# Kernel optimization log

Hardware: AMD Instinct MI355X
Metric: run time of the kernel (lower is better)

## Reference

```python
import math
import jax, jax.numpy as jnp
import numpy as np

B, S, H, M, E = 4, 4096, 1024, 1024, 16
CAPACITY_FACTOR = 2.0
ROUTE_SCALE = 1.0


def setup_inputs() -> dict:
    key = jax.random.key(0)
    ks = jax.random.split(key, 8)
    return {
        "hidden_states": jax.random.normal(ks[0], (B, S, H), dtype=jnp.float32),
        "hidden_states_unmodulated": jax.random.normal(ks[1], (B, S, H), dtype=jnp.float32),
        "timestep": jax.random.normal(ks[2], (B, H), dtype=jnp.float32),
        "gate_w": jax.random.normal(ks[3], (2 * H, E), dtype=jnp.float32) * 0.02,
        "gate_up_proj": jax.random.normal(ks[4], (E, H, 2 * M), dtype=jnp.float32) * 0.02,
        "down_proj": jax.random.normal(ks[5], (E, M, H), dtype=jnp.float32) * 0.02,
        "shared_gate_up_w": jax.random.normal(ks[6], (H, 2 * M), dtype=jnp.float32) * 0.02,
        "shared_down_w": jax.random.normal(ks[7], (M, H), dtype=jnp.float32) * 0.02,
    }


def reference(hidden_states, hidden_states_unmodulated, timestep, gate_w,
              gate_up_proj, down_proj, shared_gate_up_w, shared_down_w):
    b, s, h = hidden_states.shape
    e = gate_up_proj.shape[0]
    capacity = max(1, math.ceil(CAPACITY_FACTOR * s / e))  # static per shapes

    # --- router ---
    t = jnp.broadcast_to(timestep[:, None, :], (b, s, h))
    router_input = jnp.concatenate([t, hidden_states_unmodulated], axis=-1)  # [b,s,2h]
    logits = router_input @ gate_w                                           # [b,s,e]
    scores = jax.nn.sigmoid(logits.astype(jnp.float32)).astype(logits.dtype)
    affinity = jnp.swapaxes(scores, 1, 2)                                    # [b,e,s]

    # --- expert-choice top-k ---
    gating, top_idx = jax.lax.top_k(affinity, capacity)                      # [b,e,cap]
    offsets = (jnp.arange(b) * s)[:, None, None]
    gidx = jnp.swapaxes(offsets + top_idx, 0, 1).reshape(-1)                 # [e*b*cap]
    gflat = jnp.swapaxes(gating, 0, 1).reshape(-1)

    # normalize per-token scores over experts that picked the token
    sums = jnp.zeros(b * s, dtype=gflat.dtype).at[gidx].add(gflat)
    gflat = gflat / (sums[gidx] + 1e-12) * ROUTE_SCALE

    # --- dispatch + grouped SwiGLU experts ---
    x_flat = hidden_states.reshape(b * s, h)
    routed = x_flat[gidx].reshape(e, b * capacity, h)
    gu = jnp.einsum('eth,ehf->etf', routed, gate_up_proj)                    # [e,t,2m]
    g, u = jnp.split(gu, 2, axis=-1)
    expert_out = jnp.einsum('etm,emh->eth', jax.nn.silu(g) * u, down_proj)
    expert_out = expert_out.reshape(e * b * capacity, h)
    expert_out = (expert_out.astype(jnp.float32) *
                  gflat.astype(jnp.float32)[:, None]).astype(hidden_states.dtype)

    # --- shared expert (SwiGLUProj order: hidden * silu(gate)) ---
    hgu = hidden_states @ shared_gate_up_w                                   # [b,s,2m]
    hs_, hg = jnp.split(hgu, 2, axis=-1)
    shared = (hs_ * jax.nn.silu(hg)) @ shared_down_w                         # [b,s,h]

    # --- scatter combine ---
    out = shared.reshape(b * s, h).at[gidx].add(expert_out)
    return out.reshape(b, s, h)
```

## Files before the change

### kernel.cpp

```cpp
#include <hip/hip_runtime.h>
#include <math.h>

#define Bb 4
#define Ss 4096
#define Hh 1024
#define Mm 1024
#define Ee 16
#define CAPk 512

typedef unsigned short u16;
typedef __attribute__((ext_vector_type(8))) short short8;
typedef __attribute__((ext_vector_type(4))) float floatx4;
typedef __attribute__((ext_vector_type(4))) unsigned short ushort4v;

__device__ __forceinline__ float silu_f(float x) {
    return x / (1.0f + expf(-x));
}

__device__ __forceinline__ u16 f2b(float x) {
    union { float f; unsigned u; } v; v.f = x;
    unsigned r = (v.u + 0x7fffu + ((v.u >> 16) & 1u)) >> 16;
    return (u16)r;
}

__device__ __forceinline__ void gl_lds16(const void* g, void* l) {
    __builtin_amdgcn_global_load_lds((const __attribute__((address_space(1))) void*)g,
                                     (__attribute__((address_space(3))) void*)l, 16, 0, 0);
}


__global__ __launch_bounds__(256)
void conv_router(const float* __restrict__ hidden, u16* __restrict__ Xb,
                 const float* __restrict__ hsu,
                 const float* __restrict__ gate_w,
                 const float* __restrict__ timestep,
                 float* __restrict__ scores) {
    const int t = threadIdx.x;
    if (blockIdx.x >= 256) {
        int i = ((blockIdx.x - 256) * 256 + t) * 4;
        float4 v = *(const float4*)(hidden + i);
        ushort4v o = { f2b(v.x), f2b(v.y), f2b(v.z), f2b(v.w) };
        *(ushort4v*)(Xb + i) = o;
        return;
    }
    __shared__ float Xs[64 * 64];
    __shared__ float Gs[64 * 16];
    const int rbid = blockIdx.x;
    const int row0 = rbid * 64;
    const int b = row0 >> 12;
    const int wave = t >> 6, lane = t & 63;
    const int e0 = wave * 4;
    const float* gw2 = gate_w + (size_t)Hh * Ee;

    float tl0 = 0.f, tl1 = 0.f, tl2 = 0.f, tl3 = 0.f;
    {
        const float* tsrow = timestep + (size_t)b * Hh;
#pragma unroll
        for (int j = 0; j < 16; ++j) {
            int h = lane + 64 * j;
            float tv = tsrow[h];
            const float* gw = gate_w + (size_t)h * Ee + e0;
            tl0 += tv * gw[0]; tl1 += tv * gw[1]; tl2 += tv * gw[2]; tl3 += tv * gw[3];
        }
#pragma unroll
        for (int off = 32; off; off >>= 1) {
            tl0 += __shfl_xor(tl0, off); tl1 += __shfl_xor(tl1, off);
            tl2 += __shfl_xor(tl2, off); tl3 += __shfl_xor(tl3, off);
        }
    }

    float acc0 = 0.f, acc1 = 0.f, acc2 = 0.f, acc3 = 0.f;

    for (int k0 = 0; k0 < Hh; k0 += 64) {
        __syncthreads();
#pragma unroll
        for (int r = 0; r < 4; ++r) {
            int tok = r * 16 + (t >> 4);
            int cslot = t & 15;
            int g = cslot ^ (tok & 15);
            const float* src = hsu + (size_t)(row0 + tok) * Hh + k0 + g * 4;
            char* dst = (char*)Xs + r * 4096 + wave * 1024;
            gl_lds16(src, dst);
        }
        {
            const float* src = gw2 + (size_t)k0 * Ee + t * 4;
            char* dst = (char*)Gs + wave * 1024;
            gl_lds16(src, dst);
        }
        __syncthreads();
#pragma unroll
        for (int kk = 0; kk < 64; kk += 4) {
            int slot = (kk >> 2) ^ (lane & 15);
            float4 a = *(const float4*)&Xs[lane * 64 + slot * 4];
            float4 g0 = *(const float4*)&Gs[(kk + 0) * Ee + e0];
            float4 g1 = *(const float4*)&Gs[(kk + 1) * Ee + e0];
            float4 g2 = *(const float4*)&Gs[(kk + 2) * Ee + e0];
            float4 g3 = *(const float4*)&Gs[(kk + 3) * Ee + e0];
            acc0 += a.x * g0.x; acc0 += a.y * g1.x; acc0 += a.z * g2.x; acc0 += a.w * g3.x;
            acc1 += a.x * g0.y; acc1 += a.y * g1.y; acc1 += a.z * g2.y; acc1 += a.w * g3.y;
            acc2 += a.x * g0.z; acc2 += a.y * g1.z; acc2 += a.z * g2.z; acc2 += a.w * g3.z;
            acc3 += a.x * g0.w; acc3 += a.y * g1.w; acc3 += a.z * g2.w; acc3 += a.w * g3.w;
        }
    }
    const int s = (row0 + lane) & (Ss - 1);
    float l0 = acc0 + tl0;
    float l1 = acc1 + tl1;
    float l2 = acc2 + tl2;
    float l3 = acc3 + tl3;
    scores[((size_t)(b * Ee + e0 + 0)) * Ss + s] = 1.f / (1.f + expf(-l0));
    scores[((size_t)(b * Ee + e0 + 1)) * Ss + s] = 1.f / (1.f + expf(-l1));
    scores[((size_t)(b * Ee + e0 + 2)) * Ss + s] = 1.f / (1.f + expf(-l2));
    scores[((size_t)(b * Ee + e0 + 3)) * Ss + s] = 1.f / (1.f + expf(-l3));
}

__global__ __launch_bounds__(1024)
void topk_kernel(const float* __restrict__ scores,
                 int* __restrict__ rank) {
    const int be = blockIdx.x;
    const float* sc = scores + (size_t)be * Ss;
    int* rk = rank + (size_t)be * Ss;
    const int t = threadIdx.x;
    const int lane = t & 63, w = t >> 6;
    __shared__ unsigned hist[256];
    __shared__ unsigned wtot[16];
    __shared__ unsigned sh_prefix;
    __shared__ int sh_need;
    __shared__ unsigned cnt_gt;

#pragma unroll
    for (int i = 0; i < 4; ++i) rk[t * 4 + i] = -1;

    unsigned vu[4];
#pragma unroll
    for (int i = 0; i < 4; ++i) vu[i] = __float_as_uint(sc[t * 4 + i]);

    unsigned prefix = 0;
    int need = CAPk;
    for (int pass = 0; pass < 4; ++pass) {
        const int shift = 24 - 8 * pass;
        if (t < 256) hist[t] = 0;
        __syncthreads();
#pragma unroll
        for (int i = 0; i < 4; ++i) {
            unsigned u = vu[i];
            bool ok = (pass == 0) || ((u >> (shift + 8)) == prefix);
            if (ok) atomicAdd(&hist[(u >> shift) & 255u], 1u);
        }
        __syncthreads();
        unsigned hval = (t < 256) ? hist[t] : 0u;
        unsigned s = hval;
#pragma unroll
        for (int d = 1; d < 64; d <<= 1) {
            unsigned o = __shfl_down(s, d);
            if (lane + d < 64) s += o;
        }
        if (lane == 0 && w < 4) wtot[w] = s;
        __syncthreads();
        if (t < 256) {
#pragma unroll
            for (int w2 = 0; w2 < 4; ++w2)
                if (w2 > w) s += wtot[w2];
            unsigned Snext = s - hval;
            if (s >= (unsigned)need && Snext < (unsigned)need) {
                sh_prefix = (prefix << 8) | (unsigned)t;
                sh_need = need - (int)Snext;
            }
        }
        __syncthreads();
        prefix = sh_prefix;
        need = sh_need;
        __syncthreads();
    }
    const unsigned T = prefix;
    const int need_eq = need;
    const unsigned ngt = (unsigned)(CAPk - need_eq);

    int myeq = 0;
#pragma unroll
    for (int i = 0; i < 4; ++i) myeq += (vu[i] == T) ? 1 : 0;
    unsigned e = (unsigned)myeq;
#pragma unroll
    for (int d = 1; d < 64; d <<= 1) {
        unsigned o = __shfl_up(e, d);
        if (lane >= d) e += o;
    }
    if (lane == 63) wtot[w] = e;
    if (t == 0) cnt_gt = 0;
    __syncthreads();
    unsigned eqr = e - (unsigned)myeq;
#pragma unroll
    for (int w2 = 0; w2 < 16; ++w2)
        if (w2 < w) eqr += wtot[w2];
#pragma unroll
    for (int i = 0; i < 4; ++i) {
        unsigned u = vu[i];
        int s = t * 4 + i;
        if (u > T) {
            unsigned slot = atomicAdd(&cnt_gt, 1u);
            rk[s] = (int)slot;
        } else if (u == T) {
            if ((int)eqr < need_eq) {
                rk[s] = (int)(ngt + eqr);
            }
            eqr++;
        }
    }
}

__global__ __launch_bounds__(256)
void route_build(const float* __restrict__ scores, const int* __restrict__ rank,
                 int* __restrict__ slot_token, float* __restrict__ slot_w,
                 int* __restrict__ cnt, int* __restrict__ inv) {
    const int token = blockIdx.x * 256 + threadIdx.x;
    const int b = token >> 12, s = token & (Ss - 1);
    int rr[16];
    float gg[16];
    float sum = 0.f;
#pragma unroll
    for (int e = 0; e < 16; ++e) {
        size_t idx = (size_t)(b * Ee + e) * Ss + s;
        int r = rank[idx];
        rr[e] = r;
        float g = (r >= 0) ? scores[idx] : 0.f;
        gg[e] = g;
        sum += g;
    }
    int pos = 0;
#pragma unroll
    for (int e = 0; e < 16; ++e) {
        if (rr[e] >= 0) {
            float wv = gg[e] / (sum + 1e-12f);
            int o = (e * Bb + b) * CAPk + rr[e];
            slot_token[o] = token;
            slot_w[o] = wv;
            inv[token * 16 + pos] = o;
            ++pos;
        }
    }
    cnt[token] = pos;
}

__global__ __launch_bounds__(256)
void combine_kernel(const int* __restrict__ cnt, const int* __restrict__ inv,
                    const float* __restrict__ eo, float* __restrict__ out) {
    const int token = blockIdx.x;
    const int k = cnt[token];
    if (k == 0) return;
    const int col = threadIdx.x * 4;
    const size_t rowoff = (size_t)token * 1024 + col;
    float4 acc = *(const float4*)(out + rowoff);
    for (int j = 0; j < k; ++j) {
        int slot = inv[token * 16 + j];
        float4 v = *(const float4*)(eo + (size_t)slot * 1024 + col);
        acc.x += v.x; acc.y += v.y; acc.z += v.z; acc.w += v.w;
    }
    *(float4*)(out + rowoff) = acc;
}


__device__ __forceinline__ void tpose_body(const float* __restrict__ Ws, u16* __restrict__ Wd,
                                           int N, int n0, int k0, float tile[64][65], int t) {
    int lr = t >> 4, lc = (t & 15) * 4;
#pragma unroll
    for (int i = 0; i < 4; ++i) {
        float4 v = *(const float4*)&Ws[(size_t)(k0 + lr + i * 16) * N + n0 + lc];
        tile[lr + i * 16][lc + 0] = v.x;
        tile[lr + i * 16][lc + 1] = v.y;
        tile[lr + i * 16][lc + 2] = v.z;
        tile[lr + i * 16][lc + 3] = v.w;
    }
    __syncthreads();
    int on = t >> 2;
    int ok0 = (t & 3) * 16;
    u16 buf[16];
#pragma unroll
    for (int j = 0; j < 16; ++j) buf[j] = f2b(tile[ok0 + j][on]);
    u16* dp = &Wd[(size_t)(n0 + on) * 1024 + k0 + ok0];
    *(short8*)(dp) = *(short8*)&buf[0];
    *(short8*)(dp + 8) = *(short8*)&buf[8];
}

__global__ __launch_bounds__(256)
void transpose_bf16(const float* __restrict__ W, u16* __restrict__ Wt,
                    int N, size_t zsrc, size_t zdst) {
    __shared__ float tile[64][65];
    int n0 = blockIdx.x * 64, k0 = blockIdx.y * 64, z = blockIdx.z;
    tpose_body(W + (size_t)z * zsrc, Wt + (size_t)z * zdst, N, n0, k0, tile, threadIdx.x);
}

__global__ __launch_bounds__(256)
void transpose_all(const float* __restrict__ gate_up, const float* __restrict__ down,
                   const float* __restrict__ sh_gu, const float* __restrict__ sh_dn,
                   u16* __restrict__ Wt1r, u16* __restrict__ Wt2r,
                   u16* __restrict__ Wt1s, u16* __restrict__ Wt2s) {
    __shared__ float tile[64][65];
    const int id = blockIdx.x;
    const float* Ws; u16* Wd; int N, n0, k0;
    if (id < 8192) {
        int z = id >> 9, r = id & 511;
        n0 = (r & 31) * 64; k0 = (r >> 5) * 64; N = 2048;
        Ws = gate_up + (size_t)z * 2097152; Wd = Wt1r + (size_t)z * 2097152;
    } else if (id < 12288) {
        int i2 = id - 8192; int z = i2 >> 8, r = i2 & 255;
        n0 = (r & 15) * 64; k0 = (r >> 4) * 64; N = 1024;
        Ws = down + (size_t)z * 1048576; Wd = Wt2r + (size_t)z * 1048576;
    } else if (id < 12800) {
        int r = id - 12288;
        n0 = (r & 31) * 64; k0 = (r >> 5) * 64; N = 2048;
        Ws = sh_gu; Wd = Wt1s;
    } else {
        int r = id - 12800;
        n0 = (r & 15) * 64; k0 = (r >> 4) * 64; N = 1024;
        Ws = sh_dn; Wd = Wt2s;
    }
    tpose_body(Ws, Wd, N, n0, k0, tile, threadIdx.x);
}


__device__ __forceinline__ void stage_tile512(const u16* __restrict__ grow, int k0,
                                              u16* lds, int t) {
#pragma unroll
    for (int r = 0; r < 2; ++r) {
        int ci = r * 512 + t;
        int m = ci >> 3;
        int c = (ci & 7) ^ (m & 7);
        const u16* src = grow + (size_t)m * 1024 + k0 + c * 8;
        u16* dst = lds + ((r * 8192 + (t >> 6) * 1024) >> 1);
        gl_lds16(src, dst);
    }
}

__device__ __forceinline__ void stage_rows512(const u16* __restrict__ A, const int* rid,
                                              int k0, u16* lds, int t) {
#pragma unroll
    for (int r = 0; r < 2; ++r) {
        int ci = r * 512 + t;
        int m = ci >> 3;
        int c = (ci & 7) ^ (m & 7);
        const u16* src = A + (size_t)rid[r] * 1024 + k0 + c * 8;
        u16* dst = lds + ((r * 8192 + (t >> 6) * 1024) >> 1);
        gl_lds16(src, dst);
    }
}

template <bool SILU_FIRST, bool GATHER>
__global__ __launch_bounds__(512, 4)
void gemm1_flat(const u16* __restrict__ A,
                const u16* __restrict__ W1t, u16* __restrict__ act,
                const int* __restrict__ slot_token, int p0, int p1) {
    __shared__ u16 lA[128 * 64];
    __shared__ u16 lB1[128 * 64];
    __shared__ u16 lB2[128 * 64];
    const int t = threadIdx.x;
    const int L = blockIdx.x;
    const int x = L & 7, j = L >> 3;
    int z = 0, bm0, n0;
    if (GATHER) {
        if (p1 == 8) { z = p0 + x; bm0 = (j >> 3) << 7; }
        else         { z = p0 + (x >> 1); bm0 = (((x & 1) << 3) + (j >> 3)) << 7; }
    } else {
        bm0 = (p0 + x * (p1 >> 3) + (j >> 3)) << 7;
    }
    n0 = (j & 7) << 7;
    const int out_base = (GATHER ? z * 2048 : 0) + bm0;
    const u16* B1row = W1t + ((size_t)(GATHER ? z * 2048 : 0) + n0) * 1024;
    const u16* B2row = B1row + (size_t)1024 * 1024;
    const int lane = t & 63;
    const int wv = t >> 6;
    const int wm = wv & 1, wn = wv >> 1;
    const int quad = lane >> 4, l15 = lane & 15;

    int rid[2];
#pragma unroll
    for (int r = 0; r < 2; ++r) {
        int m = (t >> 3) + 64 * r;
        rid[r] = GATHER ? slot_token[z * (Bb * CAPk) + bm0 + m] : (bm0 + m);
    }

    floatx4 zero4 = {0.f, 0.f, 0.f, 0.f};
    floatx4 acc1[4][2], acc2[4][2];
#pragma unroll
    for (int i = 0; i < 4; ++i)
#pragma unroll
        for (int j2 = 0; j2 < 2; ++j2) { acc1[i][j2] = zero4; acc2[i][j2] = zero4; }

    for (int k0 = 0; k0 < 1024; k0 += 64) {
        __syncthreads();
        stage_rows512(A, rid, k0, lA, t);
        stage_tile512(B1row, k0, lB1, t);
        stage_tile512(B2row, k0, lB2, t);
        __syncthreads();
#pragma unroll
        for (int kc = 0; kc < 2; ++kc) {
            short8 af[4], bf1[2], bf2[2];
#pragma unroll
            for (int mi = 0; mi < 4; ++mi) {
                int m = wm * 64 + mi * 16 + l15;
                int off = m * 64 + (((kc * 4 + quad) ^ (m & 7)) * 8);
                af[mi] = *(const short8*)&lA[off];
            }
#pragma unroll
            for (int ni = 0; ni < 2; ++ni) {
                int n = wn * 32 + ni * 16 + l15;
                int off = n * 64 + (((kc * 4 + quad) ^ (n & 7)) * 8);
                bf1[ni] = *(const short8*)&lB1[off];
                bf2[ni] = *(const short8*)&lB2[off];
            }
#pragma unroll
            for (int mi = 0; mi < 4; ++mi)
#pragma unroll
                for (int ni = 0; ni < 2; ++ni) {
                    acc1[mi][ni] = __builtin_amdgcn_mfma_f32_16x16x32_bf16(af[mi], bf1[ni], acc1[mi][ni], 0, 0, 0);
                    acc2[mi][ni] = __builtin_amdgcn_mfma_f32_16x16x32_bf16(af[mi], bf2[ni], acc2[mi][ni], 0, 0, 0);
                }
        }
    }
#pragma unroll
    for (int mi = 0; mi < 4; ++mi)
#pragma unroll
        for (int ni = 0; ni < 2; ++ni)
#pragma unroll
            for (int r = 0; r < 4; ++r) {
                int m = wm * 64 + mi * 16 + quad * 4 + r;
                int n = wn * 32 + ni * 16 + l15;
                float c1 = acc1[mi][ni][r], c2 = acc2[mi][ni][r];
                float v = SILU_FIRST ? silu_f(c1) * c2 : c1 * silu_f(c2);
                act[(size_t)(out_base + m) * 1024 + n0 + n] = f2b(v);
            }
}

template <int MODE>
__global__ __launch_bounds__(512, 4)
void gemm2_flat(const u16* __restrict__ A,
                const u16* __restrict__ W2t, const float* __restrict__ slot_w,
                float* __restrict__ outp, int p0, int p1) {
    __shared__ u16 lA[128 * 64];
    __shared__ u16 lB[128 * 64];
    __shared__ float s_w[(MODE == 2) ? 128 : 1];
    const int t = threadIdx.x;
    const int L = blockIdx.x;
    const int x = L & 7, j = L >> 3;
    int z = 0, bm0, n0;
    if (MODE == 2) {
        if (p1 == 8) { z = p0 + x; bm0 = (j >> 3) << 7; }
        else         { z = p0 + (x >> 1); bm0 = (((x & 1) << 3) + (j >> 3)) << 7; }
    } else {
        bm0 = (p0 + x * (p1 >> 3) + (j >> 3)) << 7;
    }
    n0 = (j & 7) << 7;
    const int row_base = (MODE == 2 ? z * 2048 : 0) + bm0;
    const u16* Arow = A + (size_t)row_base * 1024;
    const u16* Brow = W2t + ((size_t)(MODE == 2 ? z * 1024 : 0) + n0) * 1024;
    const int lane = t & 63;
    const int wv = t >> 6;
    const int wm = wv & 1, wn = wv >> 1;
    const int quad = lane >> 4, l15 = lane & 15;

    if (MODE == 2 && t < 128) {
        s_w[t] = slot_w[row_base + t];
    }

    floatx4 zero4 = {0.f, 0.f, 0.f, 0.f};
    floatx4 acc[4][2];
#pragma unroll
    for (int i = 0; i < 4; ++i)
#pragma unroll
        for (int j2 = 0; j2 < 2; ++j2) acc[i][j2] = zero4;

    for (int k0 = 0; k0 < 1024; k0 += 64) {
        __syncthreads();
        stage_tile512(Arow, k0, lA, t);
        stage_tile512(Brow, k0, lB, t);
        __syncthreads();
#pragma unroll
        for (int kc = 0; kc < 2; ++kc) {
            short8 af[4], bf[2];
#pragma unroll
            for (int mi = 0; mi < 4; ++mi) {
                int m = wm * 64 + mi * 16 + l15;
                int off = m * 64 + (((kc * 4 + quad) ^ (m & 7)) * 8);
                af[mi] = *(const short8*)&lA[off];
            }
#pragma unroll
            for (int ni = 0; ni < 2; ++ni) {
                int n = wn * 32 + ni * 16 + l15;
                int off = n * 64 + (((kc * 4 + quad) ^ (n & 7)) * 8);
                bf[ni] = *(const short8*)&lB[off];
            }
#pragma unroll
            for (int mi = 0; mi < 4; ++mi)
#pragma unroll
                for (int ni = 0; ni < 2; ++ni)
                    acc[mi][ni] = __builtin_amdgcn_mfma_f32_16x16x32_bf16(af[mi], bf[ni], acc[mi][ni], 0, 0, 0);
        }
    }
#pragma unroll
    for (int mi = 0; mi < 4; ++mi)
#pragma unroll
        for (int ni = 0; ni < 2; ++ni)
#pragma unroll
            for (int r = 0; r < 4; ++r) {
                int m = wm * 64 + mi * 16 + quad * 4 + r;
                int n = wn * 32 + ni * 16 + l15;
                float c = acc[mi][ni][r];
                if (MODE == 2) {
                    outp[(size_t)(row_base + m) * 1024 + n0 + n] = c * s_w[m];
                } else {
                    outp[(size_t)(row_base + m) * 1024 + n0 + n] = c;
                }
            }
}


template <bool SILU_FIRST, bool GATHER>
__global__ __launch_bounds__(512, 4)
void gemm1_mfma(const u16* __restrict__ A, int a_row0, int zstride,
                const u16* __restrict__ W1t, u16* __restrict__ act,
                const int* __restrict__ slot_token, int e_base) {
    __shared__ u16 lA[128 * 64];
    __shared__ u16 lB1[128 * 64];
    __shared__ u16 lB2[128 * 64];
    const int t = threadIdx.x;
    const int n0 = blockIdx.x * 128;
    const int bm0 = blockIdx.y * 128;
    const int z = blockIdx.z;
    const int zb = z * zstride;
    const u16* B1row = W1t + ((size_t)z * 2048 + n0) * 1024;
    const u16* B2row = B1row + (size_t)1024 * 1024;
    const int lane = t & 63;
    const int wv = t >> 6;
    const int wm = wv & 1, wn = wv >> 1;
    const int quad = lane >> 4, l15 = lane & 15;

    int rid[2];
#pragma unroll
    for (int r = 0; r < 2; ++r) {
        int m = (t >> 3) + 64 * r;
        rid[r] = GATHER ? slot_token[(e_base + z) * (Bb * CAPk) + bm0 + m]
                        : (a_row0 + zb + bm0 + m);
    }

    floatx4 zero4 = {0.f, 0.f, 0.f, 0.f};
    floatx4 acc1[4][2], acc2[4][2];
#pragma unroll
    for (int i = 0; i < 4; ++i)
#pragma unroll
        for (int j = 0; j < 2; ++j) { acc1[i][j] = zero4; acc2[i][j] = zero4; }

    for (int k0 = 0; k0 < 1024; k0 += 64) {
        __syncthreads();
        stage_rows512(A, rid, k0, lA, t);
        stage_tile512(B1row, k0, lB1, t);
        stage_tile512(B2row, k0, lB2, t);
        __syncthreads();
#pragma unroll
        for (int kc = 0; kc < 2; ++kc) {
            short8 af[4], bf1[2], bf2[2];
#pragma unroll
            for (int mi = 0; mi < 4; ++mi) {
                int m = wm * 64 + mi * 16 + l15;
                int off = m * 64 + (((kc * 4 + quad) ^ (m & 7)) * 8);
                af[mi] = *(const short8*)&lA[off];
            }
#pragma unroll
            for (int ni = 0; ni < 2; ++ni) {
                int n = wn * 32 + ni * 16 + l15;
                int off = n * 64 + (((kc * 4 + quad) ^ (n & 7)) * 8);
                bf1[ni] = *(const short8*)&lB1[off];
                bf2[ni] = *(const short8*)&lB2[off];
            }
#pragma unroll
            for (int mi = 0; mi < 4; ++mi)
#pragma unroll
                for (int ni = 0; ni < 2; ++ni) {
                    acc1[mi][ni] = __builtin_amdgcn_mfma_f32_16x16x32_bf16(af[mi], bf1[ni], acc1[mi][ni], 0, 0, 0);
                    acc2[mi][ni] = __builtin_amdgcn_mfma_f32_16x16x32_bf16(af[mi], bf2[ni], acc2[mi][ni], 0, 0, 0);
                }
        }
    }
#pragma unroll
    for (int mi = 0; mi < 4; ++mi)
#pragma unroll
        for (int ni = 0; ni < 2; ++ni)
#pragma unroll
            for (int r = 0; r < 4; ++r) {
                int m = wm * 64 + mi * 16 + quad * 4 + r;
                int n = wn * 32 + ni * 16 + l15;
                float c1 = acc1[mi][ni][r], c2 = acc2[mi][ni][r];
                float v = SILU_FIRST ? silu_f(c1) * c2 : c1 * silu_f(c2);
                act[(size_t)(zb + bm0 + m) * 1024 + n0 + n] = f2b(v);
            }
}

template <int MODE>
__global__ __launch_bounds__(512, 4)
void gemm2_mfma(const u16* __restrict__ A, int zstride,
                const u16* __restrict__ W2t,
                const int* __restrict__ slot_token, const float* __restrict__ slot_w,
                float* __restrict__ out, int out_row0, int e_base) {
    __shared__ u16 lA[128 * 64];
    __shared__ u16 lB[128 * 64];
    __shared__ int s_tok[(MODE == 1) ? 128 : 1];
    __shared__ float s_w[(MODE == 1 || MODE == 2) ? 128 : 1];
    const int t = threadIdx.x;
    const int n0 = blockIdx.x * 128;
    const int bm0 = blockIdx.y * 128;
    const int z = blockIdx.z;
    const int zb = z * zstride;
    const u16* Arow = A + (size_t)(zb + bm0) * 1024;
    const u16* Brow = W2t + ((size_t)z * 1024 + n0) * 1024;
    const int lane = t & 63;
    const int wv = t >> 6;
    const int wm = wv & 1, wn = wv >> 1;
    const int quad = lane >> 4, l15 = lane & 15;

    if ((MODE == 1 || MODE == 2) && t < 128) {
        int gi = (e_base + z) * (Bb * CAPk) + bm0 + t;
        if (MODE == 1) s_tok[t] = slot_token[gi];
        s_w[t] = slot_w[gi];
    }

    floatx4 zero4 = {0.f, 0.f, 0.f, 0.f};
    floatx4 acc[4][2];
#pragma unroll
    for (int i = 0; i < 4; ++i)
#pragma unroll
        for (int j = 0; j < 2; ++j) acc[i][j] = zero4;

    for (int k0 = 0; k0 < 1024; k0 += 64) {
        __syncthreads();
        stage_tile512(Arow, k0, lA, t);
        stage_tile512(Brow, k0, lB, t);
        __syncthreads();
#pragma unroll
        for (int kc = 0; kc < 2; ++kc) {
            short8 af[4], bf[2];
#pragma unroll
            for (int mi = 0; mi < 4; ++mi) {
                int m = wm * 64 + mi * 16 + l15;
                int off = m * 64 + (((kc * 4 + quad) ^ (m & 7)) * 8);
                af[mi] = *(const short8*)&lA[off];
            }
#pragma unroll
            for (int ni = 0; ni < 2; ++ni) {
                int n = wn * 32 + ni * 16 + l15;
                int off = n * 64 + (((kc * 4 + quad) ^ (n & 7)) * 8);
                bf[ni] = *(const short8*)&lB[off];
            }
#pragma unroll
            for (int mi = 0; mi < 4; ++mi)
#pragma unroll
                for (int ni = 0; ni < 2; ++ni)
                    acc[mi][ni] = __builtin_amdgcn_mfma_f32_16x16x32_bf16(af[mi], bf[ni], acc[mi][ni], 0, 0, 0);
        }
    }
#pragma unroll
    for (int mi = 0; mi < 4; ++mi)
#pragma unroll
        for (int ni = 0; ni < 2; ++ni)
#pragma unroll
            for (int r = 0; r < 4; ++r) {
                int m = wm * 64 + mi * 16 + quad * 4 + r;
                int n = wn * 32 + ni * 16 + l15;
                float c = acc[mi][ni][r];
                if (MODE == 1) {
                    atomicAdd(&out[(size_t)s_tok[m] * 1024 + n0 + n], c * s_w[m]);
                } else if (MODE == 2) {
                    out[((size_t)((e_base + z) * (Bb * CAPk) + bm0 + m)) * 1024 + n0 + n] = c * s_w[m];
                } else {
                    out[(size_t)(out_row0 + bm0 + m) * 1024 + n0 + n] = c;
                }
            }
}


extern "C" void kernel_launch(void* const* d_in, const int* in_sizes, int n_in,
                              void* d_out, int out_size, void* d_ws, size_t ws_size,
                              hipStream_t stream) {
    const float* hidden   = (const float*)d_in[0];
    const float* hsu      = (const float*)d_in[1];
    const float* timestep = (const float*)d_in[2];
    const float* gate_w   = (const float*)d_in[3];
    const float* gate_up  = (const float*)d_in[4];
    const float* down     = (const float*)d_in[5];
    const float* sh_gu    = (const float*)d_in[6];
    const float* sh_dn    = (const float*)d_in[7];
    float* out = (float*)d_out;

    char* p = (char*)d_ws;
    auto alloc = [&](size_t bytes) { char* r = p; p += (bytes + 255) & ~(size_t)255; return r; };
    float* scores    = (float*)alloc((size_t)Bb * Ee * Ss * 4);
    int*   rank      = (int*)  alloc((size_t)Bb * Ee * Ss * 4);
    int*   slot_token= (int*)  alloc((size_t)Ee * Bb * CAPk * 4);
    float* slot_w    = (float*)alloc((size_t)Ee * Bb * CAPk * 4);
    int*   cnt       = (int*)  alloc((size_t)Bb * Ss * 4);
    int*   inv       = (int*)  alloc((size_t)Bb * Ss * 16 * 4);
    u16*   Xb        = (u16*)  alloc((size_t)16384 * 1024 * 2);
    char* phase = p;
    long long avail = (long long)((char*)d_ws + ws_size - phase);
    if (avail < 0) avail = 0;

    const long long eo_bytes     = (long long)32768 * 1024 * 4;
    const long long per_e        = ((long long)2048 * 1024 + 1024 * 1024 +
                                    (long long)2048 * 1024) * 2;
    const long long shared_fixed = ((long long)2048 * 1024 + 1024 * 1024) * 2;
    const long long fast_need    = ((long long)16 * 2048 * 1024 +
                                    (long long)16 * 1024 * 1024 +
                                    (long long)16 * 2048 * 1024 +
                                    (long long)2048 * 1024 +
                                    (long long)1024 * 1024) * 2;

    conv_router<<<16384 + (Bb * Ss) / 64, 256, 0, stream>>>(hidden, Xb, hsu, gate_w,
                                                            timestep, scores);
    topk_kernel<<<Bb * Ee, 1024, 0, stream>>>(scores, rank);
    route_build<<<(Bb * Ss) / 256, 256, 0, stream>>>(scores, rank, slot_token, slot_w,
                                                     cnt, inv);

    bool use_eo = (avail >= eo_bytes + (per_e > (shared_fixed + (long long)128 * 2048)
                                        ? per_e : (shared_fixed + (long long)128 * 2048)));
    bool fast   = use_eo && (avail - eo_bytes >= fast_need);

    if (fast) {
        float* eo = (float*)phase;
        char* ph2 = phase + eo_bytes;
        u16* Wt1r = (u16*)ph2;
        u16* Wt2r = Wt1r + (size_t)16 * 2048 * 1024;
        u16* actR = Wt2r + (size_t)16 * 1024 * 1024;
        u16* Wt1s = actR + (size_t)16 * 2048 * 1024;
        u16* Wt2s = Wt1s + (size_t)2048 * 1024;
        u16* actS = Wt1r;

        transpose_all<<<13056, 256, 0, stream>>>(gate_up, down, sh_gu, sh_dn,
                                                 Wt1r, Wt2r, Wt1s, Wt2s);
        for (int e0 = 0; e0 < 16; e0 += 4)
            gemm1_flat<true, true><<<512, 512, 0, stream>>>(
                Xb, Wt1r, actR, slot_token, e0, 4);
        gemm2_flat<2><<<1024, 512, 0, stream>>>(actR, Wt2r, slot_w, eo, 0, 8);
        gemm2_flat<2><<<1024, 512, 0, stream>>>(actR, Wt2r, slot_w, eo, 8, 8);
        gemm1_flat<false, false><<<512, 512, 0, stream>>>(
            Xb, Wt1s, actS, nullptr, 0, 64);
        gemm1_flat<false, false><<<512, 512, 0, stream>>>(
            Xb, Wt1s, actS, nullptr, 64, 64);
        gemm2_flat<0><<<512, 512, 0, stream>>>(actS, Wt2s, nullptr, out, 0, 64);
        gemm2_flat<0><<<512, 512, 0, stream>>>(actS, Wt2s, nullptr, out, 64, 64);
        combine_kernel<<<Bb * Ss, 256, 0, stream>>>(cnt, inv, eo, out);
    } else if (use_eo) {
        float* eo = (float*)phase;
        char* ph2 = phase + eo_bytes;
        long long avail2 = avail - eo_bytes;
        {
            int g = (int)(avail2 / per_e);
            if (g < 1) g = 1;
            if (g > Ee) g = Ee;
            u16* Wt1r = (u16*)ph2;
            u16* Wt2r = Wt1r + (size_t)g * 2048 * 1024;
            u16* actR = Wt2r + (size_t)g * 1024 * 1024;
            for (int e0 = 0; e0 < Ee; e0 += g) {
                int cg = Ee - e0; if (cg > g) cg = g;
                transpose_bf16<<<dim3(32, 16, cg), 256, 0, stream>>>(
                    gate_up + (size_t)e0 * 2097152, Wt1r, 2048, 2097152, 2097152);
                transpose_bf16<<<dim3(16, 16, cg), 256, 0, stream>>>(
                    down + (size_t)e0 * 1048576, Wt2r, 1024, 1048576, 1048576);
                gemm1_mfma<true, true><<<dim3(8, 16, cg), 512, 0, stream>>>(
                    Xb, 0, 2048, Wt1r, actR, slot_token, e0);
                gemm2_mfma<2><<<dim3(8, 16, cg), 512, 0, stream>>>(
                    actR, 2048, Wt2r, slot_token, slot_w, eo, 0, e0);
            }
        }
        {
            u16* Wt1s = (u16*)ph2;
            u16* Wt2s = Wt1s + (size_t)2048 * 1024;
            u16* actS = Wt2s + (size_t)1024 * 1024;
            long long room = (avail2 - shared_fixed) / 2048;
            room &= ~127LL;
            int R = (int)(room > 16384 ? 16384 : room);
            if (R < 128) R = 128;
            transpose_bf16<<<dim3(32, 16, 1), 256, 0, stream>>>(sh_gu, Wt1s, 2048, 0, 0);
            transpose_bf16<<<dim3(16, 16, 1), 256, 0, stream>>>(sh_dn, Wt2s, 1024, 0, 0);
            for (int r0 = 0; r0 < Bb * Ss; r0 += R) {
                int cur = Bb * Ss - r0; if (cur > R) cur = R;
                gemm1_mfma<false, false><<<dim3(8, cur / 128, 1), 512, 0, stream>>>(
                    Xb, r0, 0, Wt1s, actS, nullptr, 0);
                gemm2_mfma<0><<<dim3(8, cur / 128, 1), 512, 0, stream>>>(
                    actS, 0, Wt2s, nullptr, nullptr, out, r0, 0);
            }
        }
        combine_kernel<<<Bb * Ss, 256, 0, stream>>>(cnt, inv, eo, out);
    } else {
        {
            u16* Wt1s = (u16*)phase;
            u16* Wt2s = Wt1s + (size_t)2048 * 1024;
            u16* actS = Wt2s + (size_t)1024 * 1024;
            long long room = (avail - shared_fixed) / 2048;
            room &= ~127LL;
            int R = (int)(room > 16384 ? 16384 : room);
            if (R < 128) R = 128;
            transpose_bf16<<<dim3(32, 16, 1), 256, 0, stream>>>(sh_gu, Wt1s, 2048, 0, 0);
            transpose_bf16<<<dim3(16, 16, 1), 256, 0, stream>>>(sh_dn, Wt2s, 1024, 0, 0);
            for (int r0 = 0; r0 < Bb * Ss; r0 += R) {
                int cur = Bb * Ss - r0; if (cur > R) cur = R;
                gemm1_mfma<false, false><<<dim3(8, cur / 128, 1), 512, 0, stream>>>(
                    Xb, r0, 0, Wt1s, actS, nullptr, 0);
                gemm2_mfma<0><<<dim3(8, cur / 128, 1), 512, 0, stream>>>(
                    actS, 0, Wt2s, nullptr, nullptr, out, r0, 0);
            }
        }
        {
            int g = (int)(avail / per_e);
            if (g < 1) g = 1;
            if (g > Ee) g = Ee;
            u16* Wt1r = (u16*)phase;
            u16* Wt2r = Wt1r + (size_t)g * 2048 * 1024;
            u16* actR = Wt2r + (size_t)g * 1024 * 1024;
            for (int e0 = 0; e0 < Ee; e0 += g) {
                int cg = Ee - e0; if (cg > g) cg = g;
                transpose_bf16<<<dim3(32, 16, cg), 256, 0, stream>>>(
                    gate_up + (size_t)e0 * 2097152, Wt1r, 2048, 2097152, 2097152);
                transpose_bf16<<<dim3(16, 16, cg), 256, 0, stream>>>(
                    down + (size_t)e0 * 1048576, Wt2r, 1024, 1048576, 1048576);
                gemm1_mfma<true, true><<<dim3(8, 16, cg), 512, 0, stream>>>(
                    Xb, 0, 2048, Wt1r, actR, slot_token, e0);
                gemm2_mfma<1><<<dim3(8, 16, cg), 512, 0, stream>>>(
                    actR, 2048, Wt2r, slot_token, slot_w, out, 0, e0);
            }
        }
    }
}
```

Measured before the change: 796.6 us.

## Merge routed and shared expert GEMMs into single launches

Replaces the multiple partial gemm1/gemm2 launches, split by expert group or row range, with one merged gemm1 and one merged gemm2 launch of 3072 blocks each. Block index decides between the routed and shared branches. Shared activations now get their own buffer instead of aliasing Wt1r, which raises the fast-path workspace requirement. The transpose kernel is also moved ahead of topk/route_build. The goal is to cut launch overhead and fill-and-drain tails between small launches, at the cost of needing more scratch memory.

```diff
diff --git a/kernel.cpp b/kernel.cpp
--- a/kernel.cpp
+++ b/kernel.cpp
@@ -343,28 +343,41 @@
     }
 }
 
-template <bool SILU_FIRST, bool GATHER>
 __global__ __launch_bounds__(512, 4)
-void gemm1_flat(const u16* __restrict__ A,
-                const u16* __restrict__ W1t, u16* __restrict__ act,
-                const int* __restrict__ slot_token, int p0, int p1) {
+void gemm1_merged(const u16* __restrict__ Xb,
+                  const u16* __restrict__ Wt1r, const u16* __restrict__ Wt1s,
+                  u16* __restrict__ actR, u16* __restrict__ actS,
+                  const int* __restrict__ slot_token) {
     __shared__ u16 lA[128 * 64];
     __shared__ u16 lB1[128 * 64];
     __shared__ u16 lB2[128 * 64];
     const int t = threadIdx.x;
     const int L = blockIdx.x;
-    const int x = L & 7, j = L >> 3;
-    int z = 0, bm0, n0;
-    if (GATHER) {
-        if (p1 == 8) { z = p0 + x; bm0 = (j >> 3) << 7; }
-        else         { z = p0 + (x >> 1); bm0 = (((x & 1) << 3) + (j >> 3)) << 7; }
+    const bool routed = L < 2048;
+    int bm0, n0, out_base;
+    const u16 *B1, *B2;
+    u16* actp;
+    int z = 0;
+    if (routed) {
+        int x = L & 7, j = L >> 3;
+        z = x + 8 * (j >> 7);
+        int j2 = j & 127;
+        bm0 = (j2 >> 3) << 7;
+        n0 = (j2 & 7) << 7;
+        B1 = Wt1r + ((size_t)z * 2048 + n0) * 1024;
+        B2 = B1 + (size_t)1024 * 1024;
+        out_base = z * 2048 + bm0;
+        actp = actR;
     } else {
-        bm0 = (p0 + x * (p1 >> 3) + (j >> 3)) << 7;
-    }
-    n0 = (j & 7) << 7;
-    const int out_base = (GATHER ? z * 2048 : 0) + bm0;
-    const u16* B1row = W1t + ((size_t)(GATHER ? z * 2048 : 0) + n0) * 1024;
-    const u16* B2row = B1row + (size_t)1024 * 1024;
+        int l2 = L - 2048;
+        int x = l2 & 7, j = l2 >> 3;
+        bm0 = ((x << 4) + (j >> 3)) << 7;
+        n0 = (j & 7) << 7;
+        B1 = Wt1s + (size_t)n0 * 1024;
+        B2 = B1 + (size_t)1024 * 1024;
+        out_base = bm0;
+        actp = actS;
+    }
     const int lane = t & 63;
     const int wv = t >> 6;
     const int wm = wv & 1, wn = wv >> 1;
@@ -374,7 +387,7 @@
 #pragma unroll
     for (int r = 0; r < 2; ++r) {
         int m = (t >> 3) + 64 * r;
-        rid[r] = GATHER ? slot_token[z * (Bb * CAPk) + bm0 + m] : (bm0 + m);
+        rid[r] = routed ? slot_token[z * (Bb * CAPk) + bm0 + m] : (bm0 + m);
     }
 
     floatx4 zero4 = {0.f, 0.f, 0.f, 0.f};
@@ -386,9 +399,9 @@
 
     for (int k0 = 0; k0 < 1024; k0 += 64) {
         __syncthreads();
-        stage_rows512(A, rid, k0, lA, t);
-        stage_tile512(B1row, k0, lB1, t);
-        stage_tile512(B2row, k0, lB2, t);
+        stage_rows512(Xb, rid, k0, lA, t);
+        stage_tile512(B1, k0, lB1, t);
+        stage_tile512(B2, k0, lB2, t);
         __syncthreads();
 #pragma unroll
         for (int kc = 0; kc < 2; ++kc) {
@@ -424,42 +437,48 @@
                 int m = wm * 64 + mi * 16 + quad * 4 + r;
                 int n = wn * 32 + ni * 16 + l15;
                 float c1 = acc1[mi][ni][r], c2 = acc2[mi][ni][r];
-                float v = SILU_FIRST ? silu_f(c1) * c2 : c1 * silu_f(c2);
-                act[(size_t)(out_base + m) * 1024 + n0 + n] = f2b(v);
-            }
-}
-
-template <int MODE>
+                float v = routed ? silu_f(c1) * c2 : c1 * silu_f(c2);
+                actp[(size_t)(out_base + m) * 1024 + n0 + n] = f2b(v);
+            }
+}
+
 __global__ __launch_bounds__(512, 4)
-void gemm2_flat(const u16* __restrict__ A,
-                const u16* __restrict__ W2t, const float* __restrict__ slot_w,
-                float* __restrict__ outp, int p0, int p1) {
+void gemm2_merged(const u16* __restrict__ actR, const u16* __restrict__ actS,
+                  const u16* __restrict__ Wt2r, const u16* __restrict__ Wt2s,
+                  const float* __restrict__ slot_w,
+                  float* __restrict__ eo, float* __restrict__ out) {
     __shared__ u16 lA[128 * 64];
     __shared__ u16 lB[128 * 64];
-    __shared__ float s_w[(MODE == 2) ? 128 : 1];
+    __shared__ float s_w[128];
     const int t = threadIdx.x;
     const int L = blockIdx.x;
-    const int x = L & 7, j = L >> 3;
-    int z = 0, bm0, n0;
-    if (MODE == 2) {
-        if (p1 == 8) { z = p0 + x; bm0 = (j >> 3) << 7; }
-        else         { z = p0 + (x >> 1); bm0 = (((x & 1) << 3) + (j >> 3)) << 7; }
+    const bool routed = L < 2048;
+    int bm0, n0, row_base;
+    const u16 *Arow, *Brow;
+    if (routed) {
+        int x = L & 7, j = L >> 3;
+        int z = x + 8 * (j >> 7);
+        int j2 = j & 127;
+        bm0 = (j2 >> 3) << 7;
+        n0 = (j2 & 7) << 7;
+        row_base = z * 2048 + bm0;
+        Arow = actR + (size_t)row_base * 1024;
+        Brow = Wt2r + ((size_t)z * 1024 + n0) * 1024;
+        if (t < 128) s_w[t] = slot_w[row_base + t];
     } else {
-        bm0 = (p0 + x * (p1 >> 3) + (j >> 3)) << 7;
-    }
-    n0 = (j & 7) << 7;
-    const int row_base = (MODE == 2 ? z * 2048 : 0) + bm0;
-    const u16* Arow = A + (size_t)row_base * 1024;
-    const u16* Brow = W2t + ((size_t)(MODE == 2 ? z * 1024 : 0) + n0) * 1024;
+        int l2 = L - 2048;
+        int x = l2 & 7, j = l2 >> 3;
+        bm0 = ((x << 4) + (j >> 3)) << 7;
+        n0 = (j & 7) << 7;
+        row_base = bm0;
+        Arow = actS + (size_t)bm0 * 1024;
+        Brow = Wt2s + (size_t)n0 * 1024;
+    }
     const int lane = t & 63;
     const int wv = t >> 6;
     const int wm = wv & 1, wn = wv >> 1;
     const int quad = lane >> 4, l15 = lane & 15;
 
-    if (MODE == 2 && t < 128) {
-        s_w[t] = slot_w[row_base + t];
-    }
-
     floatx4 zero4 = {0.f, 0.f, 0.f, 0.f};
     floatx4 acc[4][2];
 #pragma unroll
@@ -503,10 +522,10 @@
                 int m = wm * 64 + mi * 16 + quad * 4 + r;
                 int n = wn * 32 + ni * 16 + l15;
                 float c = acc[mi][ni][r];
-                if (MODE == 2) {
-                    outp[(size_t)(row_base + m) * 1024 + n0 + n] = c * s_w[m];
+                if (routed) {
+                    eo[(size_t)(row_base + m) * 1024 + n0 + n] = c * s_w[m];
                 } else {
-                    outp[(size_t)(row_base + m) * 1024 + n0 + n] = c;
+                    out[(size_t)(row_base + m) * 1024 + n0 + n] = c;
                 }
             }
 }
@@ -707,14 +726,9 @@
     const long long fast_need    = ((long long)16 * 2048 * 1024 +
                                     (long long)16 * 1024 * 1024 +
                                     (long long)16 * 2048 * 1024 +
+                                    (long long)16384 * 1024 +
                                     (long long)2048 * 1024 +
                                     (long long)1024 * 1024) * 2;
-
-    conv_router<<<16384 + (Bb * Ss) / 64, 256, 0, stream>>>(hidden, Xb, hsu, gate_w,
-                                                            timestep, scores);
-    topk_kernel<<<Bb * Ee, 1024, 0, stream>>>(scores, rank);
-    route_build<<<(Bb * Ss) / 256, 256, 0, stream>>>(scores, rank, slot_token, slot_w,
-                                                     cnt, inv);
 
     bool use_eo = (avail >= eo_bytes + (per_e > (shared_fixed + (long long)128 * 2048)
                                         ? per_e : (shared_fixed + (long long)128 * 2048)));
@@ -726,25 +740,24 @@
         u16* Wt1r = (u16*)ph2;
         u16* Wt2r = Wt1r + (size_t)16 * 2048 * 1024;
         u16* actR = Wt2r + (size_t)16 * 1024 * 1024;
-        u16* Wt1s = actR + (size_t)16 * 2048 * 1024;
+        u16* actS = actR + (size_t)16 * 2048 * 1024;
+        u16* Wt1s = actS + (size_t)16384 * 1024;
         u16* Wt2s = Wt1s + (size_t)2048 * 1024;
-        u16* actS = Wt1r;
-
+
+        conv_router<<<16640, 256, 0, stream>>>(hidden, Xb, hsu, gate_w, timestep, scores);
         transpose_all<<<13056, 256, 0, stream>>>(gate_up, down, sh_gu, sh_dn,
                                                  Wt1r, Wt2r, Wt1s, Wt2s);
-        for (int e0 = 0; e0 < 16; e0 += 4)
-            gemm1_flat<true, true><<<512, 512, 0, stream>>>(
-                Xb, Wt1r, actR, slot_token, e0, 4);
-        gemm2_flat<2><<<1024, 512, 0, stream>>>(actR, Wt2r, slot_w, eo, 0, 8);
-        gemm2_flat<2><<<1024, 512, 0, stream>>>(actR, Wt2r, slot_w, eo, 8, 8);
-        gemm1_flat<false, false><<<512, 512, 0, stream>>>(
-            Xb, Wt1s, actS, nullptr, 0, 64);
-        gemm1_flat<false, false><<<512, 512, 0, stream>>>(
-            Xb, Wt1s, actS, nullptr, 64, 64);
-        gemm2_flat<0><<<512, 512, 0, stream>>>(actS, Wt2s, nullptr, out, 0, 64);
-        gemm2_flat<0><<<512, 512, 0, stream>>>(actS, Wt2s, nullptr, out, 64, 64);
+        topk_kernel<<<Bb * Ee, 1024, 0, stream>>>(scores, rank);
+        route_build<<<(Bb * Ss) / 256, 256, 0, stream>>>(scores, rank, slot_token, slot_w,
+                                                         cnt, inv);
+        gemm1_merged<<<3072, 512, 0, stream>>>(Xb, Wt1r, Wt1s, actR, actS, slot_token);
+        gemm2_merged<<<3072, 512, 0, stream>>>(actR, actS, Wt2r, Wt2s, slot_w, eo, out);
         combine_kernel<<<Bb * Ss, 256, 0, stream>>>(cnt, inv, eo, out);
     } else if (use_eo) {
+        conv_router<<<16640, 256, 0, stream>>>(hidden, Xb, hsu, gate_w, timestep, scores);
+        topk_kernel<<<Bb * Ee, 1024, 0, stream>>>(scores, rank);
+        route_build<<<(Bb * Ss) / 256, 256, 0, stream>>>(scores, rank, slot_token, slot_w,
+                                                         cnt, inv);
         float* eo = (float*)phase;
         char* ph2 = phase + eo_bytes;
         long long avail2 = avail - eo_bytes;
@@ -787,6 +800,10 @@
         }
         combine_kernel<<<Bb * Ss, 256, 0, stream>>>(cnt, inv, eo, out);
     } else {
+        conv_router<<<16640, 256, 0, stream>>>(hidden, Xb, hsu, gate_w, timestep, scores);
+        topk_kernel<<<Bb * Ee, 1024, 0, stream>>>(scores, rank);
+        route_build<<<(Bb * Ss) / 256, 256, 0, stream>>>(scores, rank, slot_token, slot_w,
+                                                         cnt, inv);
         {
             u16* Wt1s = (u16*)phase;
             u16* Wt2s = Wt1s + (size_t)2048 * 1024;
```

After: 756.2 us. -5.1%, faster.
